# Kernel optimization log

Hardware: AMD Instinct MI355X
Metric: run time of the kernel (lower is better)

The kernel has to match this reference:

```python
import jax, jax.numpy as jnp
import numpy as np

N_HEADS = 4
NS_STEPS = 5
NS_EPS = 1e-7

def newtonschulz5(G):
    # G: [out, in]; quintic Newton-Schulz, 5 steps. out==in here so no transpose branch needed,
    # but keep the static-shape check for faithfulness.
    a, b, c = 3.4445, -4.775, 2.0315
    X = G / (jnp.linalg.norm(G) + NS_EPS)
    transposed = G.shape[0] > G.shape[1]
    if transposed:
        X = X.T
    def step(X, _):
        A = X @ X.T
        B = b * A + c * (A @ A)
        return a * X + B @ X, None
    X, _ = jax.lax.scan(step, X, None, length=NS_STEPS)
    if transposed:
        X = X.T
    return X

def setup_inputs() -> dict:
    key = jax.random.key(0)
    k1, k2, k3, k4, k5 = jax.random.split(key, 5)
    B, S, D_in, D_out, r = 4, 2048, 4096, 4096, 16
    init_std = 0.01 / np.sqrt(D_out * r)
    return {
        "x": jax.random.normal(k1, (B, S, D_in), dtype=jnp.float32),
        "W": jax.random.normal(k2, (D_out, D_in), dtype=jnp.float32) * 0.02,
        "bias": jax.random.normal(k3, (D_out,), dtype=jnp.float32) * 0.02,
        "lora_A": jax.random.normal(k4, (r, D_in), dtype=jnp.float32),
        "lora_B": jax.random.normal(k5, (D_out, r), dtype=jnp.float32) * init_std,
    }

def reference(x, W, bias, lora_A, lora_B):
    # base linear (frozen weights); dropout is identity (p=0 / eval)
    base_out = jnp.einsum('bsi,oi->bso', x, W) + bias
    r, D_in = lora_A.shape
    D_out = lora_B.shape[0]
    hr = r // N_HEADS
    Ah = lora_A.reshape(N_HEADS, hr, D_in)                       # [h, hr, in]
    Bh = lora_B.reshape(D_out, N_HEADS, hr).transpose(1, 0, 2)    # [h, out, hr]
    G = jnp.einsum('hor,hri->hoi', Bh, Ah)                        # [h, out, in]
    alpha = jnp.sqrt(jnp.sum(G * G, axis=(1, 2)))                 # per-head Frobenius norm
    M = jax.vmap(newtonschulz5)(G)                                # [h, out, in]
    lora_out = jnp.einsum('h,hoi,bsi->bso', alpha, M, x)
    return base_out + lora_out
```

## Files before the change

### kernel.cpp

```cpp
#include <hip/hip_runtime.h>
#include <math.h>

#define MDIM 8192
#define NDIM 4096
#define KDIM 4096

typedef __attribute__((ext_vector_type(8))) _Float16 h8;
typedef __attribute__((ext_vector_type(4))) _Float16 h4;
typedef __attribute__((ext_vector_type(4))) float f32x4;

typedef const __attribute__((address_space(1))) void* gas_ptr;
typedef __attribute__((address_space(3))) void* las_ptr;

__device__ inline void load16_to_lds(const void* g, void* l) {
  __builtin_amdgcn_global_load_lds((gas_ptr)g, (las_ptr)l, 16, 0, 0);
}

__device__ inline void mm4(const double* A, const double* B, double* C) {
#pragma unroll
  for (int p = 0; p < 4; ++p)
#pragma unroll
    for (int q = 0; q < 4; ++q) {
      double s = 0.0;
#pragma unroll
      for (int r = 0; r < 4; ++r) s += A[p * 4 + r] * B[r * 4 + q];
      C[p * 4 + q] = s;
    }
}
__device__ inline void mm4_bt(const double* A, const double* B, double* C) {
#pragma unroll
  for (int p = 0; p < 4; ++p)
#pragma unroll
    for (int q = 0; q < 4; ++q) {
      double s = 0.0;
#pragma unroll
      for (int r = 0; r < 4; ++r) s += A[p * 4 + r] * B[q * 4 + r];
      C[p * 4 + q] = s;
    }
}

__global__ void ns_kernel(const float* __restrict__ lora_A,
                          const float* __restrict__ lora_B,
                          float* __restrict__ E) {
  const int h = blockIdx.x;
  const int tid = threadIdx.x;

  float gu[16], gv[16];
#pragma unroll
  for (int e = 0; e < 16; ++e) { gu[e] = 0.f; gv[e] = 0.f; }

  for (int o = tid; o < NDIM; o += 256) {
    const float4 bv = *(const float4*)(lora_B + (size_t)o * 16 + h * 4);
    const float bb[4] = {bv.x, bv.y, bv.z, bv.w};
#pragma unroll
    for (int p = 0; p < 4; ++p)
#pragma unroll
      for (int q = 0; q < 4; ++q) gu[p * 4 + q] += bb[p] * bb[q];
  }
  for (int i = tid; i < KDIM; i += 256) {
    float aa[4];
#pragma unroll
    for (int p = 0; p < 4; ++p) aa[p] = lora_A[(size_t)(h * 4 + p) * KDIM + i];
#pragma unroll
    for (int p = 0; p < 4; ++p)
#pragma unroll
      for (int q = 0; q < 4; ++q) gv[p * 4 + q] += aa[p] * aa[q];
  }

  __shared__ float red[256];
  __shared__ float Gu[16], Gv[16];
  for (int e = 0; e < 16; ++e) {
    red[tid] = gu[e];
    __syncthreads();
    for (int s = 128; s > 0; s >>= 1) {
      if (tid < s) red[tid] += red[tid + s];
      __syncthreads();
    }
    if (tid == 0) Gu[e] = red[0];
    __syncthreads();
    red[tid] = gv[e];
    __syncthreads();
    for (int s = 128; s > 0; s >>= 1) {
      if (tid < s) red[tid] += red[tid + s];
      __syncthreads();
    }
    if (tid == 0) Gv[e] = red[0];
    __syncthreads();
  }

  if (tid == 0) {
    double gud[16], gvd[16];
#pragma unroll
    for (int e = 0; e < 16; ++e) { gud[e] = Gu[e]; gvd[e] = Gv[e]; }
    double tr = 0.0;
#pragma unroll
    for (int e = 0; e < 16; ++e) tr += gud[e] * gvd[e];
    const double alpha = sqrt(tr);
    const double n0 = alpha + 1e-7;

    double C[16] = {0};
    C[0] = C[5] = C[10] = C[15] = 1.0 / n0;

    const double a = 3.4445, b = -4.775, c = 2.0315;
    for (int it = 0; it < 5; ++it) {
      double T1[16], D[16], DG[16], DGD[16], GuC[16], F[16], Cn[16];
      mm4(C, gvd, T1);
      mm4_bt(T1, C, D);
      mm4(D, gud, DG);
      mm4(DG, D, DGD);
      mm4(gud, C, GuC);
#pragma unroll
      for (int e = 0; e < 16; ++e) F[e] = b * D[e] + c * DGD[e];
      mm4(F, GuC, Cn);
#pragma unroll
      for (int e = 0; e < 16; ++e) C[e] = a * C[e] + Cn[e];
    }
#pragma unroll
    for (int e = 0; e < 16; ++e) E[h * 16 + e] = (float)(alpha * C[e]);
  }
}

__global__ void cvt_x_kernel(const float* __restrict__ x, _Float16* __restrict__ xh) {
  const size_t t = (size_t)blockIdx.x * 256 + threadIdx.x;
  const size_t base = t * 8;
  const float4 a = *(const float4*)(x + base);
  const float4 b = *(const float4*)(x + base + 4);
  h8 o;
  o[0] = (_Float16)a.x; o[1] = (_Float16)a.y; o[2] = (_Float16)a.z; o[3] = (_Float16)a.w;
  o[4] = (_Float16)b.x; o[5] = (_Float16)b.y; o[6] = (_Float16)b.z; o[7] = (_Float16)b.w;
  *(h8*)(xh + base) = o;
}

__global__ void build_weff_kernel(const float* __restrict__ W,
                                  const float* __restrict__ lora_A,
                                  const float* __restrict__ lora_B,
                                  const float* __restrict__ E,
                                  _Float16* __restrict__ Wh) {
  const int o = blockIdx.x;
  const int tid = threadIdx.x;
  __shared__ float coef[16];
  if (tid < 16) {
    const int h = tid >> 2, q = tid & 3;
    float s = 0.f;
#pragma unroll
    for (int p = 0; p < 4; ++p)
      s += lora_B[(size_t)o * 16 + h * 4 + p] * E[h * 16 + p * 4 + q];
    coef[tid] = s;
  }
  __syncthreads();
  float cf[16];
#pragma unroll
  for (int k = 0; k < 16; ++k) cf[k] = coef[k];

  for (int i = tid * 4; i < KDIM; i += 1024) {
    float4 acc = *(const float4*)(W + (size_t)o * KDIM + i);
#pragma unroll
    for (int k = 0; k < 16; ++k) {
      const float4 av = *(const float4*)(lora_A + (size_t)k * KDIM + i);
      acc.x += cf[k] * av.x; acc.y += cf[k] * av.y;
      acc.z += cf[k] * av.z; acc.w += cf[k] * av.w;
    }
    h4 pk;
    pk[0] = (_Float16)acc.x; pk[1] = (_Float16)acc.y;
    pk[2] = (_Float16)acc.z; pk[3] = (_Float16)acc.w;
    *(h4*)(Wh + (size_t)o * KDIM + i) = pk;
  }
}

__launch_bounds__(256, 2)
__global__ void gemm_kernel(const _Float16* __restrict__ Xh,
                            const _Float16* __restrict__ Wh,
                            const float* __restrict__ bias,
                            float* __restrict__ out) {
  __shared__ __align__(16) _Float16 As[128 * 32];
  __shared__ __align__(16) _Float16 Bs[128 * 32];

  const int tid = threadIdx.x;
  const int bn = blockIdx.x;
  const int bm = blockIdx.y;
  const int lane = tid & 63;
  const int wave = tid >> 6;
  const int wm = (wave >> 1) * 64;
  const int wn = (wave & 1) * 64;
  const int quad = lane >> 4;
  const int r16 = lane & 15;

  const int b0 = tid * 16;
  const int row0 = b0 >> 6;
  const int k0e = (b0 & 63) >> 1;
  const size_t Ar0 = (size_t)(bm * 128 + row0) * KDIM + k0e;
  const size_t Ar1 = (size_t)(bm * 128 + row0 + 64) * KDIM + k0e;
  const size_t Br0 = (size_t)(bn * 128 + row0) * KDIM + k0e;
  const size_t Br1 = (size_t)(bn * 128 + row0 + 64) * KDIM + k0e;

  f32x4 acc[4][4] = {};

  for (int k0 = 0; k0 < KDIM; k0 += 32) {
    __syncthreads();
    load16_to_lds(Xh + Ar0 + k0, (char*)As + b0);
    load16_to_lds(Xh + Ar1 + k0, (char*)As + b0 + 4096);
    load16_to_lds(Wh + Br0 + k0, (char*)Bs + b0);
    load16_to_lds(Wh + Br1 + k0, (char*)Bs + b0 + 4096);
    __syncthreads();

    h8 a[4], b[4];
#pragma unroll
    for (int i = 0; i < 4; ++i) {
      a[i] = *(const h8*)(As + (wm + i * 16 + r16) * 32 + quad * 8);
      b[i] = *(const h8*)(Bs + (wn + i * 16 + r16) * 32 + quad * 8);
    }
#pragma unroll
    for (int i = 0; i < 4; ++i)
#pragma unroll
      for (int j = 0; j < 4; ++j)
        acc[i][j] = __builtin_amdgcn_mfma_f32_16x16x32_f16(a[i], b[j], acc[i][j], 0, 0, 0);
  }

  const int orow = bm * 128 + wm + quad * 4;
  const int ocol = bn * 128 + wn + r16;
#pragma unroll
  for (int j = 0; j < 4; ++j) {
    const int cc = ocol + j * 16;
    const float bv = bias[cc];
#pragma unroll
    for (int i = 0; i < 4; ++i) {
#pragma unroll
      for (int rg = 0; rg < 4; ++rg) {
        const int rr = orow + i * 16 + rg;
        out[(size_t)rr * NDIM + cc] = acc[i][j][rg] + bv;
      }
    }
  }
}

extern "C" void kernel_launch(void* const* d_in, const int* in_sizes, int n_in,
                              void* d_out, int out_size, void* d_ws, size_t ws_size,
                              hipStream_t stream) {
  const float* x      = (const float*)d_in[0];
  const float* W      = (const float*)d_in[1];
  const float* bias   = (const float*)d_in[2];
  const float* lora_A = (const float*)d_in[3];
  const float* lora_B = (const float*)d_in[4];
  float* out = (float*)d_out;

  char* ws = (char*)d_ws;
  float* E = (float*)ws;
  _Float16* Wh = (_Float16*)(ws + 1024);
  _Float16* Xh = (_Float16*)(ws + 1024 + (size_t)NDIM * KDIM * 2);

  ns_kernel<<<dim3(4), dim3(256), 0, stream>>>(lora_A, lora_B, E);
  cvt_x_kernel<<<dim3((MDIM * KDIM) / (256 * 8)), dim3(256), 0, stream>>>(x, Xh);
  build_weff_kernel<<<dim3(NDIM), dim3(256), 0, stream>>>(W, lora_A, lora_B, E, Wh);
  gemm_kernel<<<dim3(NDIM / 128, MDIM / 128), dim3(256), 0, stream>>>(Xh, Wh, bias, out);
}
```

Measured before the change: 666.6 us.

## Swizzle GEMM LDS layout, fuse prep kernels, use wave shuffles in NS reduction

The GEMM's global-to-LDS loads now place 16-byte chunks with an XOR swizzle on the k-chunk index, and the MFMA operand reads use the matching swizzle. This is meant to cut LDS bank conflicts on the h8 fragment reads. The x conversion and effective-weight build are merged into one launch, which saves a kernel launch and lets the two run concurrently. The NS kernel replaces its serial shared-memory tree reductions with wave shuffles plus a 4-way combine.

```diff
diff --git a/kernel.cpp b/kernel.cpp
--- a/kernel.cpp
+++ b/kernel.cpp
@@ -44,6 +44,8 @@
                           float* __restrict__ E) {
   const int h = blockIdx.x;
   const int tid = threadIdx.x;
+  const int lane = tid & 63;
+  const int wave = tid >> 6;
 
   float gu[16], gv[16];
 #pragma unroll
@@ -67,31 +69,28 @@
       for (int q = 0; q < 4; ++q) gv[p * 4 + q] += aa[p] * aa[q];
   }
 
-  __shared__ float red[256];
-  __shared__ float Gu[16], Gv[16];
+#pragma unroll
   for (int e = 0; e < 16; ++e) {
-    red[tid] = gu[e];
-    __syncthreads();
-    for (int s = 128; s > 0; s >>= 1) {
-      if (tid < s) red[tid] += red[tid + s];
-      __syncthreads();
-    }
-    if (tid == 0) Gu[e] = red[0];
-    __syncthreads();
-    red[tid] = gv[e];
-    __syncthreads();
-    for (int s = 128; s > 0; s >>= 1) {
-      if (tid < s) red[tid] += red[tid + s];
-      __syncthreads();
-    }
-    if (tid == 0) Gv[e] = red[0];
-    __syncthreads();
-  }
+#pragma unroll
+    for (int off = 32; off > 0; off >>= 1) {
+      gu[e] += __shfl_down(gu[e], off, 64);
+      gv[e] += __shfl_down(gv[e], off, 64);
+    }
+  }
+  __shared__ float pu[4][16], pv[4][16];
+  if (lane == 0) {
+#pragma unroll
+    for (int e = 0; e < 16; ++e) { pu[wave][e] = gu[e]; pv[wave][e] = gv[e]; }
+  }
+  __syncthreads();
 
   if (tid == 0) {
     double gud[16], gvd[16];
 #pragma unroll
-    for (int e = 0; e < 16; ++e) { gud[e] = Gu[e]; gvd[e] = Gv[e]; }
+    for (int e = 0; e < 16; ++e) {
+      gud[e] = (double)pu[0][e] + pu[1][e] + pu[2][e] + pu[3][e];
+      gvd[e] = (double)pv[0][e] + pv[1][e] + pv[2][e] + pv[3][e];
+    }
     double tr = 0.0;
 #pragma unroll
     for (int e = 0; e < 16; ++e) tr += gud[e] * gvd[e];
@@ -120,50 +119,52 @@
   }
 }
 
-__global__ void cvt_x_kernel(const float* __restrict__ x, _Float16* __restrict__ xh) {
-  const size_t t = (size_t)blockIdx.x * 256 + threadIdx.x;
-  const size_t base = t * 8;
-  const float4 a = *(const float4*)(x + base);
-  const float4 b = *(const float4*)(x + base + 4);
-  h8 o;
-  o[0] = (_Float16)a.x; o[1] = (_Float16)a.y; o[2] = (_Float16)a.z; o[3] = (_Float16)a.w;
-  o[4] = (_Float16)b.x; o[5] = (_Float16)b.y; o[6] = (_Float16)b.z; o[7] = (_Float16)b.w;
-  *(h8*)(xh + base) = o;
-}
-
-__global__ void build_weff_kernel(const float* __restrict__ W,
-                                  const float* __restrict__ lora_A,
-                                  const float* __restrict__ lora_B,
-                                  const float* __restrict__ E,
-                                  _Float16* __restrict__ Wh) {
-  const int o = blockIdx.x;
+__global__ void prep_kernel(const float* __restrict__ x,
+                            const float* __restrict__ W,
+                            const float* __restrict__ lora_A,
+                            const float* __restrict__ lora_B,
+                            const float* __restrict__ E,
+                            _Float16* __restrict__ Wh,
+                            _Float16* __restrict__ Xh) {
   const int tid = threadIdx.x;
-  __shared__ float coef[16];
-  if (tid < 16) {
-    const int h = tid >> 2, q = tid & 3;
-    float s = 0.f;
-#pragma unroll
-    for (int p = 0; p < 4; ++p)
-      s += lora_B[(size_t)o * 16 + h * 4 + p] * E[h * 16 + p * 4 + q];
-    coef[tid] = s;
-  }
-  __syncthreads();
-  float cf[16];
-#pragma unroll
-  for (int k = 0; k < 16; ++k) cf[k] = coef[k];
-
-  for (int i = tid * 4; i < KDIM; i += 1024) {
-    float4 acc = *(const float4*)(W + (size_t)o * KDIM + i);
-#pragma unroll
-    for (int k = 0; k < 16; ++k) {
-      const float4 av = *(const float4*)(lora_A + (size_t)k * KDIM + i);
-      acc.x += cf[k] * av.x; acc.y += cf[k] * av.y;
-      acc.z += cf[k] * av.z; acc.w += cf[k] * av.w;
-    }
-    h4 pk;
-    pk[0] = (_Float16)acc.x; pk[1] = (_Float16)acc.y;
-    pk[2] = (_Float16)acc.z; pk[3] = (_Float16)acc.w;
-    *(h4*)(Wh + (size_t)o * KDIM + i) = pk;
+  if (blockIdx.x < NDIM) {
+    const int o = blockIdx.x;
+    __shared__ float coef[16];
+    if (tid < 16) {
+      const int h = tid >> 2, q = tid & 3;
+      float s = 0.f;
+#pragma unroll
+      for (int p = 0; p < 4; ++p)
+        s += lora_B[(size_t)o * 16 + h * 4 + p] * E[h * 16 + p * 4 + q];
+      coef[tid] = s;
+    }
+    __syncthreads();
+    float cf[16];
+#pragma unroll
+    for (int k = 0; k < 16; ++k) cf[k] = coef[k];
+
+    for (int i = tid * 4; i < KDIM; i += 1024) {
+      float4 acc = *(const float4*)(W + (size_t)o * KDIM + i);
+#pragma unroll
+      for (int k = 0; k < 16; ++k) {
+        const float4 av = *(const float4*)(lora_A + (size_t)k * KDIM + i);
+        acc.x += cf[k] * av.x; acc.y += cf[k] * av.y;
+        acc.z += cf[k] * av.z; acc.w += cf[k] * av.w;
+      }
+      h4 pk;
+      pk[0] = (_Float16)acc.x; pk[1] = (_Float16)acc.y;
+      pk[2] = (_Float16)acc.z; pk[3] = (_Float16)acc.w;
+      *(h4*)(Wh + (size_t)o * KDIM + i) = pk;
+    }
+  } else {
+    const size_t t = (size_t)(blockIdx.x - NDIM) * 256 + tid;
+    const size_t base = t * 8;
+    const float4 a = *(const float4*)(x + base);
+    const float4 b = *(const float4*)(x + base + 4);
+    h8 o;
+    o[0] = (_Float16)a.x; o[1] = (_Float16)a.y; o[2] = (_Float16)a.z; o[3] = (_Float16)a.w;
+    o[4] = (_Float16)b.x; o[5] = (_Float16)b.y; o[6] = (_Float16)b.z; o[7] = (_Float16)b.w;
+    *(h8*)(Xh + base) = o;
   }
 }
 
@@ -185,29 +186,34 @@
   const int quad = lane >> 4;
   const int r16 = lane & 15;
 
-  const int b0 = tid * 16;
-  const int row0 = b0 >> 6;
-  const int k0e = (b0 & 63) >> 1;
-  const size_t Ar0 = (size_t)(bm * 128 + row0) * KDIM + k0e;
-  const size_t Ar1 = (size_t)(bm * 128 + row0 + 64) * KDIM + k0e;
-  const size_t Br0 = (size_t)(bn * 128 + row0) * KDIM + k0e;
-  const size_t Br1 = (size_t)(bn * 128 + row0 + 64) * KDIM + k0e;
+  const int c0 = tid;
+  const int c1 = tid + 256;
+  const int row0 = c0 >> 2, row1 = c1 >> 2;
+  const int col0 = ((c0 & 3) ^ ((row0 >> 1) & 3)) * 8;
+  const int col1 = ((c1 & 3) ^ ((row1 >> 1) & 3)) * 8;
+  const size_t Ar0 = (size_t)(bm * 128 + row0) * KDIM + col0;
+  const size_t Ar1 = (size_t)(bm * 128 + row1) * KDIM + col1;
+  const size_t Br0 = (size_t)(bn * 128 + row0) * KDIM + col0;
+  const size_t Br1 = (size_t)(bn * 128 + row1) * KDIM + col1;
+  const int ldsb = tid * 16;
 
   f32x4 acc[4][4] = {};
 
   for (int k0 = 0; k0 < KDIM; k0 += 32) {
     __syncthreads();
-    load16_to_lds(Xh + Ar0 + k0, (char*)As + b0);
-    load16_to_lds(Xh + Ar1 + k0, (char*)As + b0 + 4096);
-    load16_to_lds(Wh + Br0 + k0, (char*)Bs + b0);
-    load16_to_lds(Wh + Br1 + k0, (char*)Bs + b0 + 4096);
+    load16_to_lds(Xh + Ar0 + k0, (char*)As + ldsb);
+    load16_to_lds(Xh + Ar1 + k0, (char*)As + ldsb + 4096);
+    load16_to_lds(Wh + Br0 + k0, (char*)Bs + ldsb);
+    load16_to_lds(Wh + Br1 + k0, (char*)Bs + ldsb + 4096);
     __syncthreads();
 
     h8 a[4], b[4];
 #pragma unroll
     for (int i = 0; i < 4; ++i) {
-      a[i] = *(const h8*)(As + (wm + i * 16 + r16) * 32 + quad * 8);
-      b[i] = *(const h8*)(Bs + (wn + i * 16 + r16) * 32 + quad * 8);
+      const int ra = wm + i * 16 + r16;
+      const int rb = wn + i * 16 + r16;
+      a[i] = *(const h8*)(As + ra * 32 + ((quad ^ ((ra >> 1) & 3)) * 8));
+      b[i] = *(const h8*)(Bs + rb * 32 + ((quad ^ ((rb >> 1) & 3)) * 8));
     }
 #pragma unroll
     for (int i = 0; i < 4; ++i)
@@ -249,7 +255,7 @@
   _Float16* Xh = (_Float16*)(ws + 1024 + (size_t)NDIM * KDIM * 2);
 
   ns_kernel<<<dim3(4), dim3(256), 0, stream>>>(lora_A, lora_B, E);
-  cvt_x_kernel<<<dim3((MDIM * KDIM) / (256 * 8)), dim3(256), 0, stream>>>(x, Xh);
-  build_weff_kernel<<<dim3(NDIM), dim3(256), 0, stream>>>(W, lora_A, lora_B, E, Wh);
+  prep_kernel<<<dim3(NDIM + (MDIM * KDIM) / (256 * 8)), dim3(256), 0, stream>>>(
+      x, W, lora_A, lora_B, E, Wh, Xh);
   gemm_kernel<<<dim3(NDIM / 128, MDIM / 128), dim3(256), 0, stream>>>(Xh, Wh, bias, out);
 }
```

Result: faster. 645.7 us (-3.1%).
